# Performance work log

Measured on AMD Instinct MI355X. Metric: run time of the kernel, lower is better.

## Reference

```python
import jax, jax.numpy as jnp
import numpy as np


def setup_inputs() -> dict:
    key = jax.random.key(0)
    k1, k2, k3 = jax.random.split(key, 3)
    B, V, J = 32, 100000, 52
    vertices = jax.random.normal(k1, (1, V, 3), dtype=jnp.float32)
    lbs_weights = jax.random.uniform(k2, (1, V, J), dtype=jnp.float32)
    skinning_transforms = jax.random.normal(k3, (B, J, 4, 4), dtype=jnp.float32)
    return {
        "vertices": vertices,
        "lbs_weights": lbs_weights,
        "skinning_transforms": skinning_transforms,
    }


def reference(vertices, lbs_weights, skinning_transforms):
    # 3D-vertices branch of Skinning.forward
    B = skinning_transforms.shape[0]
    J = skinning_transforms.shape[1]
    V = vertices.shape[1]
    # W: [B,V,J] (broadcast of [1,V,J]); T_flat: [B,V,16] -> T: [B,V,4,4]
    T = jnp.einsum(
        "bvj,bjx->bvx",
        jnp.broadcast_to(lbs_weights, (B, V, J)),
        skinning_transforms.reshape(B, J, 16),
    ).reshape(B, V, 4, 4)
    # homogeneous vertex coords [B,V,4]
    v_posed_homo = jnp.concatenate(
        [
            jnp.broadcast_to(vertices, (B, V, 3)),
            jnp.ones((B, V, 1), dtype=vertices.dtype),
        ],
        axis=2,
    )
    # per-vertex 4x4 @ 4 transform, keep xyz
    v_homo = jnp.einsum("bvij,bvj->bvi", T, v_posed_homo)
    return v_homo[:, :, :3]
```

## Files before the change

kernel.cpp:

```cpp
#include <hip/hip_runtime.h>
#include <hip/hip_bf16.h>


typedef __attribute__((ext_vector_type(8))) short bf16x8;
typedef __attribute__((ext_vector_type(4))) float f32x4;

constexpr int J      = 52;
constexpr int KSTEPS = 7;
constexpr int NT     = 6;
constexpr int WAVES  = 4;
constexpr int MT     = 2;
constexpr int VPW    = MT * 16;
constexpr int VPB    = WAVES * VPW;
constexpr int NSLOT  = KSTEPS * NT * 64;
constexpr int BP_B   = NSLOT * 16;

typedef const __attribute__((address_space(1))) char* gas1_t;
typedef __attribute__((address_space(3))) char* las3_t;

__device__ __forceinline__ unsigned pk2(float a, float b) {
    __hip_bfloat162 h = __float22bfloat162_rn(make_float2(a, b));
    return *reinterpret_cast<unsigned*>(&h);
}

__global__ __launch_bounds__(256) void pack_A(
    const float* __restrict__ xf,
    bf16x8* __restrict__ Bp)
{
    const int slot = blockIdx.x * 256 + threadIdx.x;
    if (slot >= NSLOT) return;
    const int s    = slot / (NT * 64);
    const int rem  = slot - s * (NT * 64);
    const int t    = rem >> 6;
    const int l    = rem & 63;
    const int lgrp = l >> 4;
    const int lrow = l & 15;
    const int n = t * 16 + lrow;
    const int b = n / 3;
    const int i = n - 3 * b;
    const int j0 = s * 8 + lgrp * 2;
    const float4* __restrict__ xf4 = reinterpret_cast<const float4*>(xf);
    float4 m0 = {0,0,0,0}, m1 = {0,0,0,0};
    if (j0 < J)     m0 = xf4[(b * J + j0) * 4 + i];
    if (j0 + 1 < J) m1 = xf4[(b * J + j0 + 1) * 4 + i];
    union { bf16x8 v; unsigned w[4]; } r;
    r.w[0] = pk2(m0.x, m0.y); r.w[1] = pk2(m0.z, m0.w);
    r.w[2] = pk2(m1.x, m1.y); r.w[3] = pk2(m1.z, m1.w);
    Bp[slot] = r.v;
}

__global__ __launch_bounds__(256) void skin_mfma(
    const float* __restrict__ verts,
    const float* __restrict__ weights,
    const bf16x8* __restrict__ Bp,
    float* __restrict__ out,
    int V)
{
    __shared__ __align__(16) char sBp[BP_B];

    const int tid  = threadIdx.x;
    const int lane = tid & 63;
    const int wid  = tid >> 6;
    const int lgrp = lane >> 4;
    const int lrow = lane & 15;
    const int v0   = blockIdx.x * VPB;

    {
        const char* g = (const char*)Bp;
        for (int p = wid; p < BP_B / 1024; p += WAVES) {
            __builtin_amdgcn_global_load_lds(
                (gas1_t)(g + p * 1024 + lane * 16),
                (las3_t)(sBp + p * 1024), 16, 0, 0);
        }
    }

    int   vv[MT];
    bool  vok[MT];
    float hx[MT], hy[MT], hz[MT];
    float2 wv[MT][KSTEPS];
#pragma unroll
    for (int mt = 0; mt < MT; ++mt) {
        const int v = v0 + wid * VPW + mt * 16 + lrow;
        vv[mt]  = v;
        vok[mt] = (v < V);
        const int vcl = vok[mt] ? v : (V - 1);
        hx[mt] = verts[3 * (size_t)vcl + 0];
        hy[mt] = verts[3 * (size_t)vcl + 1];
        hz[mt] = verts[3 * (size_t)vcl + 2];
        const float* wr = weights + (size_t)vcl * J;
#pragma unroll
        for (int s = 0; s < KSTEPS; ++s) {
            const int j0 = s * 8 + lgrp * 2;
            wv[mt][s] = (j0 < J) ? *(const float2*)(wr + j0) : float2{0.f, 0.f};
        }
    }

    __syncthreads();

    f32x4 acc[MT][NT];
#pragma unroll
    for (int mt = 0; mt < MT; ++mt)
#pragma unroll
        for (int t = 0; t < NT; ++t)
            acc[mt][t] = f32x4{0.f, 0.f, 0.f, 0.f};

#pragma unroll
    for (int s = 0; s < KSTEPS; ++s) {
        bf16x8 frag[NT];
#pragma unroll
        for (int t = 0; t < NT; ++t)
            frag[t] = *(const bf16x8*)(sBp + ((s * NT + t) * 64 + lane) * 16);
#pragma unroll
        for (int mt = 0; mt < MT; ++mt) {
            const float w0 = wv[mt][s].x, w1 = wv[mt][s].y;
            union { bf16x8 v; unsigned w[4]; } xf8;
            xf8.w[0] = pk2(w0 * hx[mt], w0 * hy[mt]);
            xf8.w[1] = pk2(w0 * hz[mt], w0);
            xf8.w[2] = pk2(w1 * hx[mt], w1 * hy[mt]);
            xf8.w[3] = pk2(w1 * hz[mt], w1);
#pragma unroll
            for (int t = 0; t < NT; ++t) {
                acc[mt][t] = __builtin_amdgcn_mfma_f32_16x16x32_bf16(
                    frag[t], xf8.v, acc[mt][t], 0, 0, 0);
            }
        }
    }

#pragma unroll
    for (int mt = 0; mt < MT; ++mt) {
        if (!vok[mt]) continue;
        const size_t v3 = (size_t)vv[mt] * 3;
#pragma unroll
        for (int t = 0; t < NT; ++t) {
#pragma unroll
            for (int r = 0; r < 4; ++r) {
                const int n = 16 * t + lgrp * 4 + r;
                const int b = n / 3;
                const int i = n - 3 * b;
                out[(size_t)b * (size_t)V * 3 + v3 + i] = acc[mt][t][r];
            }
        }
    }
}

extern "C" void kernel_launch(void* const* d_in, const int* in_sizes, int n_in,
                              void* d_out, int out_size, void* d_ws, size_t ws_size,
                              hipStream_t stream)
{
    const float* verts   = (const float*)d_in[0];
    const float* weights = (const float*)d_in[1];
    const float* xf      = (const float*)d_in[2];
    float* out = (float*)d_out;

    const int V = in_sizes[0] / 3;
    bf16x8* Bp = (bf16x8*)d_ws;

    pack_A<<<(NSLOT + 255) / 256, 256, 0, stream>>>(xf, Bp);
    const int nblocks = (V + VPB - 1) / VPB;
    skin_mfma<<<nblocks, 256, 0, stream>>>(verts, weights, Bp, out, V);
}
```

Before: 29.03 us.

## Stage output through LDS for coalesced float4 stores

Measured after the change: 25.90 us. 1.12x faster.

```diff
diff --git a/kernel.cpp b/kernel.cpp
--- a/kernel.cpp
+++ b/kernel.cpp
@@ -14,6 +14,7 @@
 constexpr int VPB    = WAVES * VPW;
 constexpr int NSLOT  = KSTEPS * NT * 64;
 constexpr int BP_B   = NSLOT * 16;
+constexpr int OUT_B  = 16 * VPB * 3 * 4;
 
 typedef const __attribute__((address_space(1))) char* gas1_t;
 typedef __attribute__((address_space(3))) char* las3_t;
@@ -49,7 +50,7 @@
     Bp[slot] = r.v;
 }
 
-__global__ __launch_bounds__(256) void skin_mfma(
+__global__ __launch_bounds__(256, 2) void skin_mfma(
     const float* __restrict__ verts,
     const float* __restrict__ weights,
     const bf16x8* __restrict__ Bp,
@@ -57,6 +58,7 @@
     int V)
 {
     __shared__ __align__(16) char sBp[BP_B];
+    __shared__ __align__(16) char sOut[OUT_B];
 
     const int tid  = threadIdx.x;
     const int lane = tid & 63;
@@ -74,16 +76,12 @@
         }
     }
 
-    int   vv[MT];
-    bool  vok[MT];
     float hx[MT], hy[MT], hz[MT];
     float2 wv[MT][KSTEPS];
 #pragma unroll
     for (int mt = 0; mt < MT; ++mt) {
-        const int v = v0 + wid * VPW + mt * 16 + lrow;
-        vv[mt]  = v;
-        vok[mt] = (v < V);
-        const int vcl = vok[mt] ? v : (V - 1);
+        const int v   = v0 + wid * VPW + mt * 16 + lrow;
+        const int vcl = (v < V) ? v : (V - 1);
         hx[mt] = verts[3 * (size_t)vcl + 0];
         hy[mt] = verts[3 * (size_t)vcl + 1];
         hz[mt] = verts[3 * (size_t)vcl + 2];
@@ -126,18 +124,38 @@
         }
     }
 
+    const long long validf = ((long long)V - v0) * 3;
 #pragma unroll
-    for (int mt = 0; mt < MT; ++mt) {
-        if (!vok[mt]) continue;
-        const size_t v3 = (size_t)vv[mt] * 3;
+    for (int h = 0; h < 2; ++h) {
+        __syncthreads();
 #pragma unroll
-        for (int t = 0; t < NT; ++t) {
+        for (int mt = 0; mt < MT; ++mt) {
+            const int vloc = wid * VPW + mt * 16 + lrow;
 #pragma unroll
-            for (int r = 0; r < 4; ++r) {
-                const int n = 16 * t + lgrp * 4 + r;
-                const int b = n / 3;
-                const int i = n - 3 * b;
-                out[(size_t)b * (size_t)V * 3 + v3 + i] = acc[mt][t][r];
+            for (int tt = 0; tt < 3; ++tt) {
+                const int t = 3 * h + tt;
+#pragma unroll
+                for (int r = 0; r < 4; ++r) {
+                    const int n  = 16 * t + lgrp * 4 + r;
+                    const int b  = n / 3;
+                    const int i  = n - 3 * b;
+                    const int fl = ((b - 16 * h) * VPB + vloc) * 3 + i;
+                    *(float*)(sOut + fl * 4) = acc[mt][t][r];
+                }
+            }
+        }
+        __syncthreads();
+#pragma unroll
+        for (int q = 0; q < 6; ++q) {
+            const int idx = q * 256 + tid;
+            const int bl  = idx / 96;
+            const int rr  = idx - bl * 96;
+            const f32x4 val = *(const f32x4*)(sOut + (bl * 96 + rr) * 16);
+            if ((long long)rr * 4 + 4 <= validf) {
+                const int b = 16 * h + bl;
+                float4* dst = (float4*)(out + (size_t)b * (size_t)V * 3
+                                            + (size_t)v0 * 3) + rr;
+                *dst = *(const float4*)&val;
             }
         }
     }
```
